# Kernel tuning notes

Measured on AMD Instinct MI355X. Metric: run time of the kernel, lower is better.

Reference implementation:

```python
import jax, jax.numpy as jnp
import numpy as np

B, C, H, W = 16, 512, 64, 64
L, D = 77, 768
NH = 8
HD = C // NH
EPS = 1e-5


def layernorm(x, g, b):
    m = jnp.mean(x, axis=-1, keepdims=True)
    v = jnp.var(x, axis=-1, keepdims=True)
    return (x - m) * jax.lax.rsqrt(v + EPS) * g + b


def setup_inputs() -> dict:
    key = jax.random.key(0)
    ks = jax.random.split(key, 12)
    s_c = 1.0 / np.sqrt(C)
    s_d = 1.0 / np.sqrt(D)
    return {
        "x": jax.random.normal(ks[0], (B, C, H, W), jnp.float32),
        "text_features": jax.random.normal(ks[1], (B, L, D), jnp.float32),
        "wq": jax.random.normal(ks[2], (C, C), jnp.float32) * s_c,
        "bq": jnp.zeros((C,), jnp.float32),
        "wk": jax.random.normal(ks[3], (C, D), jnp.float32) * s_d,
        "bk": jnp.zeros((C,), jnp.float32),
        "wv": jax.random.normal(ks[4], (C, D), jnp.float32) * s_d,
        "bv": jnp.zeros((C,), jnp.float32),
        "wo": jax.random.normal(ks[5], (C, C), jnp.float32) * s_c,
        "bo": jnp.zeros((C,), jnp.float32),
        "g1": jnp.ones((C,), jnp.float32),
        "b1": jnp.zeros((C,), jnp.float32),
        "g2": jnp.ones((C,), jnp.float32),
        "b2": jnp.zeros((C,), jnp.float32),
    }


def reference(x, text_features, wq, bq, wk, bk, wv, bv, wo, bo, g1, b1, g2, b2):
    b, c, h, w = x.shape
    # 1x1 conv query projection
    q = jnp.einsum('bchw,oc->bohw', x, wq) + bq[None, :, None, None]
    # 2D positional encoding: first c/2 channels vary along w, next c/2 along h
    pos_x = jnp.broadcast_to(jnp.linspace(0.0, 1.0, w)[None, :], (h, w))
    pos_y = jnp.broadcast_to(jnp.linspace(0.0, 1.0, h)[:, None], (h, w))
    pe = jnp.concatenate([
        jnp.broadcast_to(pos_x[None], (c // 2, h, w)),
        jnp.broadcast_to(pos_y[None], (c // 2, h, w)),
    ], axis=0)  # [C,H,W]
    q = q + 0.05 * pe[None]
    # flatten spatial -> tokens, layernorm over channels
    q_flat = q.reshape(b, c, h * w).transpose(0, 2, 1)  # [B,HW,C]
    q_norm = layernorm(q_flat, g1, b1)
    qh = q_norm.reshape(b, h * w, NH, HD)  # [B,HW,NH,HD]
    # text key/value projections
    k = jnp.einsum('bld,cd->blc', text_features, wk) + bk
    v = jnp.einsum('bld,cd->blc', text_features, wv) + bv
    k_norm = layernorm(k, g2, b2)
    kh = k_norm.reshape(b, -1, NH, HD)
    vh = v.reshape(b, -1, NH, HD)
    scale = HD ** -0.5
    attn = jnp.einsum('bqhd,bkhd->bhqk', qh, kh) * scale  # [B,NH,HW,L]
    attn = jax.nn.softmax(attn, axis=-1)  # dropout is identity in eval
    out = jnp.einsum('bhqk,bkhd->bqhd', attn, vh).reshape(b, h * w, c)
    out = out.transpose(0, 2, 1).reshape(b, c, h, w)
    out = jnp.einsum('bchw,oc->bohw', out, wo) + bo[None, :, None, None]
    return out + x
```

## Files before the change

kernel.cpp:

```cpp
#include <hip/hip_runtime.h>
#include <stdint.h>

#define BD   16
#define CD   512
#define HD_  64
#define NH_  8
#define HWD  4096
#define LD   77
#define DD   768

typedef __bf16 bf16;
typedef bf16 bf16x8 __attribute__((ext_vector_type(8)));
typedef float f32x4 __attribute__((ext_vector_type(4)));

__device__ __forceinline__ void async16(const bf16* g, bf16* l) {
  __builtin_amdgcn_global_load_lds(
      (const __attribute__((address_space(1))) void*)g,
      (__attribute__((address_space(3))) void*)l, 16, 0, 0);
}

__device__ __forceinline__ unsigned short bfb(float f) {
  bf16 h = (bf16)f;
  return __builtin_bit_cast(unsigned short, h);
}

__global__ __launch_bounds__(256) void xpose_cvt(const float* __restrict__ X,
                                                 bf16* __restrict__ Y) {
  __shared__ float tile[64][68];
  const int b = blockIdx.z, c0 = blockIdx.y * 64, t0 = blockIdx.x * 64;
  const int tid = threadIdx.x;
  const float* Xb = X + ((size_t)b * CD + c0) * HWD + t0;
#pragma unroll
  for (int p = 0; p < 4; ++p) {
    int c = (tid >> 4) + p * 16;
    int t = (tid & 15) * 4;
    float4 v = *(const float4*)(Xb + (size_t)c * HWD + t);
    *(float4*)&tile[c][t] = v;
  }
  __syncthreads();
  int t = tid >> 2, cb = (tid & 3) * 16;
  union { uint4 u[2]; unsigned short us[16]; } pk;
#pragma unroll
  for (int j = 0; j < 16; ++j) pk.us[j] = bfb(tile[cb + j][t]);
  uint4* Yp = (uint4*)(Y + ((size_t)(b * HWD + t0 + t)) * CD + c0 + cb);
  Yp[0] = pk.u[0];
  Yp[1] = pk.u[1];
}

__global__ __launch_bounds__(256) void cvt_all(
    const float* __restrict__ t, const float* __restrict__ q,
    const float* __restrict__ k, const float* __restrict__ v,
    const float* __restrict__ o, bf16* __restrict__ tb, bf16* __restrict__ qb,
    bf16* __restrict__ kb, bf16* __restrict__ vb, bf16* __restrict__ ob) {
  int bid = blockIdx.x;
  const float* src;
  bf16* dst;
  if (bid < 462) { src = t; dst = tb; }
  else if (bid < 590) { src = q; dst = qb; bid -= 462; }
  else if (bid < 782) { src = k; dst = kb; bid -= 590; }
  else if (bid < 974) { src = v; dst = vb; bid -= 782; }
  else { src = o; dst = ob; bid -= 974; }
  int i = (bid * 256 + threadIdx.x) * 8;
  float4 a = *(const float4*)(src + i);
  float4 c = *(const float4*)(src + i + 4);
  union { uint4 u; unsigned short us[8]; } pk;
  pk.us[0] = bfb(a.x); pk.us[1] = bfb(a.y); pk.us[2] = bfb(a.z); pk.us[3] = bfb(a.w);
  pk.us[4] = bfb(c.x); pk.us[5] = bfb(c.y); pk.us[6] = bfb(c.z); pk.us[7] = bfb(c.w);
  *(uint4*)(dst + i) = pk.u;
}

template <int TM, int TN, int MODE, int NBX>
__global__ __launch_bounds__(256)
void gemm_bt(const bf16* __restrict__ A, const bf16* __restrict__ B,
             int M, int N, int K,
             const float* __restrict__ bias, const float* __restrict__ xres,
             float* __restrict__ D,
             const bf16* __restrict__ B2, const float* __restrict__ bias2,
             float* __restrict__ D2) {
  constexpr int WM = TM / 2, WN = TN / 2;
  constexpr int AFR = WM / 16, BFR = WN / 16;
  constexpr int ACH = TM / 8, TCH = (TM + TN) / 8, WCH = TCH / 4;
  static_assert(WCH == 8, "vmcnt(8) literal assumes 8 loads/wave/tile");
  __shared__ bf16 sA[2][TM * 64];
  __shared__ bf16 sB[2][TN * 64];
  const int tid = threadIdx.x, wave = tid >> 6, lane = tid & 63;
  int flat = blockIdx.x;
  {
    const int qq = (int)gridDim.x >> 3;
    flat = (flat & 7) * qq + (flat >> 3);
  }
  const int m0 = (flat / NBX) * TM;
  int n0 = (flat % NBX) * TN;
  if constexpr (MODE == 2) {
    if (n0 >= (N >> 1)) { B = B2; bias = bias2; D = D2; n0 -= (N >> 1); }
  }
  const int wm = (wave >> 1) * WM, wn = (wave & 1) * WN;
  const int sub = lane >> 3, col8 = (lane & 7) * 8;
  const int mlo = lane & 15, khi = lane >> 4;
  f32x4 acc[AFR][BFR] = {};

  auto stage = [&](int buf, int k0) {
#pragma unroll
    for (int r = 0; r < WCH; ++r) {
      int ci = wave * WCH + r;
      if (ci < ACH) {
        int row = ci * 8 + sub;
        int g = m0 + row;
        if (g > M - 1) g = M - 1;
        async16(A + (size_t)g * K + k0 + col8, &sA[buf][ci * 512]);
      } else {
        int cj = ci - ACH;
        int row = cj * 8 + sub;
        async16(B + (size_t)(n0 + row) * K + k0 + col8, &sB[buf][cj * 512]);
      }
    }
  };

  const int NT = K >> 6;
  stage(0, 0);
  stage(1, 64);
  asm volatile("s_waitcnt vmcnt(8)" ::: "memory");
  __builtin_amdgcn_s_barrier();
  __builtin_amdgcn_sched_barrier(0);

  for (int t = 0; t < NT; ++t) {
    const int cur = t & 1;
#pragma unroll
    for (int kc = 0; kc < 2; ++kc) {
      bf16x8 af[AFR], bfv[BFR];
      const int ko = kc * 32 + khi * 8;
#pragma unroll
      for (int i = 0; i < AFR; ++i)
        af[i] = *(const bf16x8*)&sA[cur][(wm + i * 16 + mlo) * 64 + ko];
#pragma unroll
      for (int j = 0; j < BFR; ++j)
        bfv[j] = *(const bf16x8*)&sB[cur][(wn + j * 16 + mlo) * 64 + ko];
#pragma unroll
      for (int i = 0; i < AFR; ++i)
#pragma unroll
        for (int j = 0; j < BFR; ++j)
          acc[i][j] = __builtin_amdgcn_mfma_f32_16x16x32_bf16(af[i], bfv[j],
                                                              acc[i][j], 0, 0, 0);
    }
    asm volatile("s_waitcnt lgkmcnt(0)" ::: "memory");
    __builtin_amdgcn_s_barrier();
    if (t + 2 < NT) {
      stage(cur, (t + 2) << 6);
      asm volatile("s_waitcnt vmcnt(8)" ::: "memory");
      __builtin_amdgcn_s_barrier();
      __builtin_amdgcn_sched_barrier(0);
    } else if (t + 1 < NT) {
      asm volatile("s_waitcnt vmcnt(0)" ::: "memory");
      __builtin_amdgcn_s_barrier();
      __builtin_amdgcn_sched_barrier(0);
    }
  }

  if constexpr (MODE == 0) {
    __shared__ float sRS[TM][2][2];
    bf16* Dq = (bf16*)D;
    const int wnh = wave & 1;
#pragma unroll
    for (int i = 0; i < AFR; ++i) {
#pragma unroll
      for (int r = 0; r < 4; ++r) {
        const int rowt = wm + i * 16 + khi * 4 + r;
        const int m = m0 + rowt;
        const int hw = m & (HWD - 1);
        const float pex = (float)(hw & 63) * (0.05f / 63.0f);
        const float pey = (float)(hw >> 6) * (0.05f / 63.0f);
        float s = 0.f, sq = 0.f;
#pragma unroll
        for (int j = 0; j < BFR; ++j) {
          const int n = n0 + wn + j * 16 + mlo;
          float v = acc[i][j][r] + bias[n] + (n < 256 ? pex : pey);
          bf16 hv = (bf16)v;
          Dq[(size_t)m * CD + n] = hv;
          float vr = (float)hv;
          s += vr;
          sq += vr * vr;
        }
        s += __shfl_xor(s, 1); sq += __shfl_xor(sq, 1);
        s += __shfl_xor(s, 2); sq += __shfl_xor(sq, 2);
        s += __shfl_xor(s, 4); sq += __shfl_xor(sq, 4);
        s += __shfl_xor(s, 8); sq += __shfl_xor(sq, 8);
        if (mlo == 0) { sRS[rowt][wnh][0] = s; sRS[rowt][wnh][1] = sq; }
      }
    }
    __syncthreads();
    if (tid < TM) {
      float s = sRS[tid][0][0] + sRS[tid][1][0];
      float sq = sRS[tid][0][1] + sRS[tid][1][1];
      float2* pst = (float2*)xres;
      pst[(size_t)(n0 >> 7) * (BD * HWD) + (m0 + tid)] = make_float2(s, sq);
    }
  } else if constexpr (MODE == 3) {
    float bn[BFR];
#pragma unroll
    for (int j = 0; j < BFR; ++j) bn[j] = bias[n0 + wn + j * 16 + mlo];
#pragma unroll
    for (int i = 0; i < AFR; ++i) {
      const int m = m0 + wm + i * 16 + khi * 4;
      const int b = m >> 12, hw = m & (HWD - 1);
      const float* xr0 = xres + ((size_t)b * CD) * HWD + hw;
      float* d0 = D + ((size_t)b * CD) * HWD + hw;
#pragma unroll
      for (int j = 0; j < BFR; ++j) {
        const size_t off = (size_t)(n0 + wn + j * 16 + mlo) * HWD;
        float4 xr = *(const float4*)(xr0 + off);
        float4 ov;
        ov.x = acc[i][j][0] + bn[j] + xr.x;
        ov.y = acc[i][j][1] + bn[j] + xr.y;
        ov.z = acc[i][j][2] + bn[j] + xr.z;
        ov.w = acc[i][j][3] + bn[j] + xr.w;
        *(float4*)(d0 + off) = ov;
      }
    }
  } else {
#pragma unroll
    for (int i = 0; i < AFR; ++i) {
      const int mb = m0 + wm + i * 16 + khi * 4;
#pragma unroll
      for (int j = 0; j < BFR; ++j) {
        const int n = n0 + wn + j * 16 + mlo;
#pragma unroll
        for (int r = 0; r < 4; ++r) {
          const int m = mb + r;
          if (m < M) D[(size_t)m * CD + n] = acc[i][j][r] + bias[n];
        }
      }
    }
  }
}

__global__ __launch_bounds__(256) void ln_rows(const float* __restrict__ X,
                                               const float* __restrict__ gg,
                                               const float* __restrict__ bb,
                                               bf16* __restrict__ Y, int nrows,
                                               int khlayout) {
  const int wv = threadIdx.x >> 6, lane = threadIdx.x & 63;
  const int row = blockIdx.x * 4 + wv;
  if (row >= nrows) return;
  const float* xr = X + (size_t)row * CD + lane * 8;
  float4 v0 = *(const float4*)xr;
  float4 v1 = *(const float4*)(xr + 4);
  float xv[8] = {v0.x, v0.y, v0.z, v0.w, v1.x, v1.y, v1.z, v1.w};
  float s = 0.f, sq = 0.f;
#pragma unroll
  for (int j = 0; j < 8; ++j) { s += xv[j]; sq += xv[j] * xv[j]; }
#pragma unroll
  for (int off = 1; off < 64; off <<= 1) {
    s += __shfl_xor(s, off);
    sq += __shfl_xor(sq, off);
  }
  float mean = s * (1.0f / 512.0f);
  float var = sq * (1.0f / 512.0f) - mean * mean;
  float rstd = rsqrtf(var + 1e-5f);
  const int c0 = lane * 8;
  union { uint4 u; unsigned short us[8]; } pk;
#pragma unroll
  for (int j = 0; j < 8; ++j)
    pk.us[j] = bfb((xv[j] - mean) * rstd * gg[c0 + j] + bb[c0 + j]);
  size_t ya;
  if (khlayout) {
    int bq = row / LD, l = row - bq * LD;
    int hh = lane >> 3, dd = (lane & 7) * 8;
    ya = (((size_t)(bq * NH_ + hh)) * LD + l) * HD_ + dd;
  } else {
    ya = (size_t)row * CD + c0;
  }
  *(uint4*)(Y + ya) = pk.u;
}

__global__ __launch_bounds__(256) void make_vt(const float* __restrict__ vraw,
                                               bf16* __restrict__ vt) {
  const int bh = blockIdx.x, b = bh >> 3, h = bh & 7;
  const int tid = threadIdx.x, d = tid & 63, lg = tid >> 6;
  for (int l = lg; l < 96; l += 4) {
    float v = 0.f;
    if (l < LD) v = vraw[((size_t)(b * LD + l)) * CD + h * HD_ + d];
    vt[((size_t)(bh * HD_ + d)) * 96 + l] = (bf16)v;
  }
}

__global__ __launch_bounds__(256) void attn_k(const bf16* __restrict__ Q,
                                              const float2* __restrict__ PST,
                                              const float* __restrict__ G1,
                                              const float* __restrict__ B1,
                                              const bf16* __restrict__ KH,
                                              const bf16* __restrict__ VT,
                                              bf16* __restrict__ O) {
  __shared__ bf16 P[4][16 * 104];
  const int tid = threadIdx.x, wv = tid >> 6, lane = tid & 63;
  const int m = lane & 15, kg = lane >> 4;
  const int q0 = blockIdx.x * 64, h = blockIdx.y, b = blockIdx.z;
  const int bh = b * NH_ + h;

  const int rowg = b * HWD + q0 + wv * 16 + m;
  const size_t qoff = (size_t)rowg * CD + h * HD_;
  bf16x8 a0r = *(const bf16x8*)(Q + qoff + kg * 8);
  bf16x8 a1r = *(const bf16x8*)(Q + qoff + 32 + kg * 8);

  float2 st = PST[(size_t)kg * (BD * HWD) + rowg];
  float s = st.x, sq = st.y;
  s += __shfl_xor(s, 16); sq += __shfl_xor(sq, 16);
  s += __shfl_xor(s, 32); sq += __shfl_xor(sq, 32);
  const float mean = s * (1.0f / 512.0f);
  const float var = sq * (1.0f / 512.0f) - mean * mean;
  const float rstd = rsqrtf(var + 1e-5f);

  const int c0 = h * HD_ + kg * 8;
  float4 ga = *(const float4*)(G1 + c0), gb = *(const float4*)(G1 + c0 + 4);
  float4 gc = *(const float4*)(G1 + c0 + 32), gd = *(const float4*)(G1 + c0 + 36);
  float4 ta = *(const float4*)(B1 + c0), tb = *(const float4*)(B1 + c0 + 4);
  float4 tc = *(const float4*)(B1 + c0 + 32), td = *(const float4*)(B1 + c0 + 36);
  const float gg[16] = {ga.x, ga.y, ga.z, ga.w, gb.x, gb.y, gb.z, gb.w,
                        gc.x, gc.y, gc.z, gc.w, gd.x, gd.y, gd.z, gd.w};
  const float bbv[16] = {ta.x, ta.y, ta.z, ta.w, tb.x, tb.y, tb.z, tb.w,
                         tc.x, tc.y, tc.z, tc.w, td.x, td.y, td.z, td.w};
  bf16x8 a0, a1;
#pragma unroll
  for (int e = 0; e < 8; ++e) {
    a0[e] = (bf16)(((float)a0r[e] - mean) * rstd * gg[e] + bbv[e]);
    a1[e] = (bf16)(((float)a1r[e] - mean) * rstd * gg[8 + e] + bbv[8 + e]);
  }

  const bf16* Kb = KH + (size_t)bh * LD * HD_;
  f32x4 sacc[5];
#pragma unroll
  for (int kt = 0; kt < 5; ++kt) {
    int key = kt * 16 + m;
    if (key > LD - 1) key = LD - 1;
    const bf16* kr = Kb + key * HD_ + kg * 8;
    bf16x8 b0 = *(const bf16x8*)kr;
    bf16x8 b1 = *(const bf16x8*)(kr + 32);
    f32x4 z = {0.f, 0.f, 0.f, 0.f};
    z = __builtin_amdgcn_mfma_f32_16x16x32_bf16(a0, b0, z, 0, 0, 0);
    z = __builtin_amdgcn_mfma_f32_16x16x32_bf16(a1, b1, z, 0, 0, 0);
    sacc[kt] = z;
  }

  bf16* Pw = &P[wv][0];
#pragma unroll
  for (int r = 0; r < 4; ++r) {
    float sc[5];
#pragma unroll
    for (int kt = 0; kt < 5; ++kt) {
      float v = sacc[kt][r] * 0.125f;
      if (kt == 4 && m >= LD - 64) v = -3.0e38f;
      sc[kt] = v;
    }
    float mx = fmaxf(fmaxf(fmaxf(sc[0], sc[1]), fmaxf(sc[2], sc[3])), sc[4]);
    mx = fmaxf(mx, __shfl_xor(mx, 1));
    mx = fmaxf(mx, __shfl_xor(mx, 2));
    mx = fmaxf(mx, __shfl_xor(mx, 4));
    mx = fmaxf(mx, __shfl_xor(mx, 8));
    float sum = 0.f;
#pragma unroll
    for (int kt = 0; kt < 5; ++kt) {
      sc[kt] = __expf(sc[kt] - mx);
      sum += sc[kt];
    }
    sum += __shfl_xor(sum, 1);
    sum += __shfl_xor(sum, 2);
    sum += __shfl_xor(sum, 4);
    sum += __shfl_xor(sum, 8);
    float inv = 1.0f / sum;
    const int prow = kg * 4 + r;
#pragma unroll
    for (int kt = 0; kt < 5; ++kt)
      Pw[prow * 104 + kt * 16 + m] = (bf16)(sc[kt] * inv);
    Pw[prow * 104 + 80 + m] = (bf16)0.f;
  }
  __syncthreads();

  bf16x8 ap[3];
#pragma unroll
  for (int kc = 0; kc < 3; ++kc)
    ap[kc] = *(const bf16x8*)&Pw[m * 104 + kc * 32 + kg * 8];

  const bf16* Vb = VT + (size_t)bh * HD_ * 96;
  f32x4 o[4] = {};
#pragma unroll
  for (int nt = 0; nt < 4; ++nt) {
#pragma unroll
    for (int kc = 0; kc < 3; ++kc) {
      bf16x8 bv = *(const bf16x8*)(Vb + (nt * 16 + m) * 96 + kc * 32 + kg * 8);
      o[nt] = __builtin_amdgcn_mfma_f32_16x16x32_bf16(ap[kc], bv, o[nt], 0, 0, 0);
    }
  }
#pragma unroll
  for (int nt = 0; nt < 4; ++nt)
#pragma unroll
    for (int r = 0; r < 4; ++r) {
      const int row = b * HWD + q0 + wv * 16 + kg * 4 + r;
      O[(size_t)row * CD + h * HD_ + nt * 16 + m] = (bf16)(o[nt][r]);
    }
}

extern "C" void kernel_launch(void* const* d_in, const int* in_sizes, int n_in,
                              void* d_out, int out_size, void* d_ws, size_t ws_size,
                              hipStream_t stream) {
  const float* x    = (const float*)d_in[0];
  const float* text = (const float*)d_in[1];
  const float* wq   = (const float*)d_in[2];
  const float* bq   = (const float*)d_in[3];
  const float* wk   = (const float*)d_in[4];
  const float* bk   = (const float*)d_in[5];
  const float* wv   = (const float*)d_in[6];
  const float* bv   = (const float*)d_in[7];
  const float* wo   = (const float*)d_in[8];
  const float* bo   = (const float*)d_in[9];
  const float* g1   = (const float*)d_in[10];
  const float* b1   = (const float*)d_in[11];
  const float* g2   = (const float*)d_in[12];
  const float* b2   = (const float*)d_in[13];
  float* out = (float*)d_out;

  char* p = (char*)d_ws;
  auto alloc = [&](size_t bytes) {
    char* r = p;
    p += (bytes + 255) & ~(size_t)255;
    return r;
  };
  bf16* xt     = (bf16*)alloc((size_t)BD * HWD * CD * 2);
  bf16* attn_o = (bf16*)alloc((size_t)BD * HWD * CD * 2);
  bf16* textb  = (bf16*)alloc((size_t)BD * LD * DD * 2);
  bf16* wqb    = (bf16*)alloc((size_t)CD * CD * 2);
  bf16* wkb    = (bf16*)alloc((size_t)CD * DD * 2);
  bf16* wvb    = (bf16*)alloc((size_t)CD * DD * 2);
  bf16* wob    = (bf16*)alloc((size_t)CD * CD * 2);
  float* kraw  = (float*)alloc((size_t)BD * LD * CD * 4);
  float* vraw  = (float*)alloc((size_t)BD * LD * CD * 4);
  bf16* kh     = (bf16*)alloc((size_t)BD * NH_ * LD * HD_ * 2);
  bf16* vt     = (bf16*)alloc((size_t)BD * NH_ * HD_ * 96 * 2);
  float* pstat = (float*)alloc((size_t)4 * BD * HWD * 2 * 4);
  bf16* qbf = (bf16*)out;

  xpose_cvt<<<dim3(HWD / 64, CD / 64, BD), 256, 0, stream>>>(x, xt);
  cvt_all<<<1102, 256, 0, stream>>>(text, wq, wk, wv, wo,
                                    textb, wqb, wkb, wvb, wob);

  gemm_bt<128, 128, 2, 8><<<80, 256, 0, stream>>>(
      textb, wkb, BD * LD, 2 * CD, DD, bk, nullptr, kraw, wvb, bv, vraw);
  ln_rows<<<(BD * LD + 3) / 4, 256, 0, stream>>>(kraw, g2, b2, kh, BD * LD, 1);
  make_vt<<<BD * NH_, 256, 0, stream>>>(vraw, vt);

  gemm_bt<128, 128, 0, 4><<<2048, 256, 0, stream>>>(
      xt, wqb, BD * HWD, CD, CD, bq, pstat, (float*)qbf,
      nullptr, nullptr, nullptr);

  attn_k<<<dim3(HWD / 64, NH_, BD), 256, 0, stream>>>(
      qbf, (const float2*)pstat, g1, b1, kh, vt, attn_o);

  gemm_bt<128, 128, 3, 4><<<2048, 256, 0, stream>>>(
      attn_o, wob, BD * HWD, CD, CD, bo, x, out, nullptr, nullptr, nullptr);
}
```

Measured before the change: 539.5 us.

## Swizzle GEMM LDS tiles, precompute load pointers, fuse V transpose into GEMM epilogue

```diff
diff --git a/kernel.cpp b/kernel.cpp
--- a/kernel.cpp
+++ b/kernel.cpp
@@ -81,8 +81,7 @@
   constexpr int AFR = WM / 16, BFR = WN / 16;
   constexpr int ACH = TM / 8, TCH = (TM + TN) / 8, WCH = TCH / 4;
   static_assert(WCH == 8, "vmcnt(8) literal assumes 8 loads/wave/tile");
-  __shared__ bf16 sA[2][TM * 64];
-  __shared__ bf16 sB[2][TN * 64];
+  __shared__ bf16 sM[2][(TM + TN) * 64];
   const int tid = threadIdx.x, wave = tid >> 6, lane = tid & 63;
   int flat = blockIdx.x;
   {
@@ -91,61 +90,76 @@
   }
   const int m0 = (flat / NBX) * TM;
   int n0 = (flat % NBX) * TN;
+  bool vside = false;
   if constexpr (MODE == 2) {
-    if (n0 >= (N >> 1)) { B = B2; bias = bias2; D = D2; n0 -= (N >> 1); }
+    if (n0 >= (N >> 1)) { B = B2; bias = bias2; vside = true; n0 -= (N >> 1); }
   }
   const int wm = (wave >> 1) * WM, wn = (wave & 1) * WN;
   const int sub = lane >> 3, col8 = (lane & 7) * 8;
+  const int csw = col8 ^ (sub * 8);
   const int mlo = lane & 15, khi = lane >> 4;
+  const int rxor = (mlo & 7) * 8;
   f32x4 acc[AFR][BFR] = {};
 
-  auto stage = [&](int buf, int k0) {
-#pragma unroll
-    for (int r = 0; r < WCH; ++r) {
-      int ci = wave * WCH + r;
-      if (ci < ACH) {
-        int row = ci * 8 + sub;
-        int g = m0 + row;
-        if (g > M - 1) g = M - 1;
-        async16(A + (size_t)g * K + k0 + col8, &sA[buf][ci * 512]);
-      } else {
-        int cj = ci - ACH;
-        int row = cj * 8 + sub;
-        async16(B + (size_t)(n0 + row) * K + k0 + col8, &sB[buf][cj * 512]);
-      }
-    }
+  const bf16* gp[WCH];
+  int ldoff[WCH];
+#pragma unroll
+  for (int r = 0; r < WCH; ++r) {
+    int ci = wave * WCH + r;
+    if (ci < ACH) {
+      int g = m0 + ci * 8 + sub;
+      if (g > M - 1) g = M - 1;
+      gp[r] = A + (size_t)g * K + csw;
+      ldoff[r] = ci * 512;
+    } else {
+      int cj = ci - ACH;
+      gp[r] = B + (size_t)(n0 + cj * 8 + sub) * K + csw;
+      ldoff[r] = TM * 64 + cj * 512;
+    }
+  }
+
+  auto stage = [&](int buf, int t) {
+    const int k0 = t << 6;
+#pragma unroll
+    for (int r = 0; r < WCH; ++r)
+      async16(gp[r] + k0, &sM[buf][ldoff[r]]);
   };
 
   const int NT = K >> 6;
   stage(0, 0);
-  stage(1, 64);
+  stage(1, 1);
   asm volatile("s_waitcnt vmcnt(8)" ::: "memory");
   __builtin_amdgcn_s_barrier();
   __builtin_amdgcn_sched_barrier(0);
 
   for (int t = 0; t < NT; ++t) {
     const int cur = t & 1;
+    const bf16* sA = &sM[cur][0];
+    const bf16* sB = &sM[cur][TM * 64];
 #pragma unroll
     for (int kc = 0; kc < 2; ++kc) {
       bf16x8 af[AFR], bfv[BFR];
       const int ko = kc * 32 + khi * 8;
+      const int kos = ko ^ rxor;
 #pragma unroll
       for (int i = 0; i < AFR; ++i)
-        af[i] = *(const bf16x8*)&sA[cur][(wm + i * 16 + mlo) * 64 + ko];
+        af[i] = *(const bf16x8*)&sA[(wm + i * 16 + mlo) * 64 + kos];
 #pragma unroll
       for (int j = 0; j < BFR; ++j)
-        bfv[j] = *(const bf16x8*)&sB[cur][(wn + j * 16 + mlo) * 64 + ko];
+        bfv[j] = *(const bf16x8*)&sB[(wn + j * 16 + mlo) * 64 + kos];
+      __builtin_amdgcn_s_setprio(1);
 #pragma unroll
       for (int i = 0; i < AFR; ++i)
 #pragma unroll
         for (int j = 0; j < BFR; ++j)
           acc[i][j] = __builtin_amdgcn_mfma_f32_16x16x32_bf16(af[i], bfv[j],
                                                               acc[i][j], 0, 0, 0);
+      __builtin_amdgcn_s_setprio(0);
     }
     asm volatile("s_waitcnt lgkmcnt(0)" ::: "memory");
     __builtin_amdgcn_s_barrier();
     if (t + 2 < NT) {
-      stage(cur, (t + 2) << 6);
+      stage(cur, t + 2);
       asm volatile("s_waitcnt vmcnt(8)" ::: "memory");
       __builtin_amdgcn_s_barrier();
       __builtin_amdgcn_sched_barrier(0);
@@ -217,6 +231,7 @@
       }
     }
   } else {
+    bf16* vt = (bf16*)D2;
 #pragma unroll
     for (int i = 0; i < AFR; ++i) {
       const int mb = m0 + wm + i * 16 + khi * 4;
@@ -226,7 +241,16 @@
 #pragma unroll
         for (int r = 0; r < 4; ++r) {
           const int m = mb + r;
-          if (m < M) D[(size_t)m * CD + n] = acc[i][j][r] + bias[n];
+          if (m < M) {
+            float v = acc[i][j][r] + bias[n];
+            if (!vside) {
+              D[(size_t)m * CD + n] = v;
+            } else {
+              const int b = m / LD, l = m - b * LD;
+              const int h = n >> 6, d = n & 63;
+              vt[(((size_t)(b * NH_ + h)) * HD_ + d) * 96 + l] = (bf16)v;
+            }
+          }
         }
       }
     }
@@ -236,8 +260,7 @@
 __global__ __launch_bounds__(256) void ln_rows(const float* __restrict__ X,
                                                const float* __restrict__ gg,
                                                const float* __restrict__ bb,
-                                               bf16* __restrict__ Y, int nrows,
-                                               int khlayout) {
+                                               bf16* __restrict__ Y, int nrows) {
   const int wv = threadIdx.x >> 6, lane = threadIdx.x & 63;
   const int row = blockIdx.x * 4 + wv;
   if (row >= nrows) return;
@@ -261,26 +284,10 @@
 #pragma unroll
   for (int j = 0; j < 8; ++j)
     pk.us[j] = bfb((xv[j] - mean) * rstd * gg[c0 + j] + bb[c0 + j]);
-  size_t ya;
-  if (khlayout) {
-    int bq = row / LD, l = row - bq * LD;
-    int hh = lane >> 3, dd = (lane & 7) * 8;
-    ya = (((size_t)(bq * NH_ + hh)) * LD + l) * HD_ + dd;
-  } else {
-    ya = (size_t)row * CD + c0;
-  }
+  int bq = row / LD, l = row - bq * LD;
+  int hh = lane >> 3, dd = (lane & 7) * 8;
+  size_t ya = (((size_t)(bq * NH_ + hh)) * LD + l) * HD_ + dd;
   *(uint4*)(Y + ya) = pk.u;
-}
-
-__global__ __launch_bounds__(256) void make_vt(const float* __restrict__ vraw,
-                                               bf16* __restrict__ vt) {
-  const int bh = blockIdx.x, b = bh >> 3, h = bh & 7;
-  const int tid = threadIdx.x, d = tid & 63, lg = tid >> 6;
-  for (int l = lg; l < 96; l += 4) {
-    float v = 0.f;
-    if (l < LD) v = vraw[((size_t)(b * LD + l)) * CD + h * HD_ + d];
-    vt[((size_t)(bh * HD_ + d)) * 96 + l] = (bf16)v;
-  }
 }
 
 __global__ __launch_bounds__(256) void attn_k(const bf16* __restrict__ Q,
@@ -431,20 +438,19 @@
   bf16* wvb    = (bf16*)alloc((size_t)CD * DD * 2);
   bf16* wob    = (bf16*)alloc((size_t)CD * CD * 2);
   float* kraw  = (float*)alloc((size_t)BD * LD * CD * 4);
-  float* vraw  = (float*)alloc((size_t)BD * LD * CD * 4);
   bf16* kh     = (bf16*)alloc((size_t)BD * NH_ * LD * HD_ * 2);
   bf16* vt     = (bf16*)alloc((size_t)BD * NH_ * HD_ * 96 * 2);
   float* pstat = (float*)alloc((size_t)4 * BD * HWD * 2 * 4);
   bf16* qbf = (bf16*)out;
 
+  hipMemsetAsync(vt, 0, (size_t)BD * NH_ * HD_ * 96 * 2, stream);
   xpose_cvt<<<dim3(HWD / 64, CD / 64, BD), 256, 0, stream>>>(x, xt);
   cvt_all<<<1102, 256, 0, stream>>>(text, wq, wk, wv, wo,
                                     textb, wqb, wkb, wvb, wob);
 
   gemm_bt<128, 128, 2, 8><<<80, 256, 0, stream>>>(
-      textb, wkb, BD * LD, 2 * CD, DD, bk, nullptr, kraw, wvb, bv, vraw);
-  ln_rows<<<(BD * LD + 3) / 4, 256, 0, stream>>>(kraw, g2, b2, kh, BD * LD, 1);
-  make_vt<<<BD * NH_, 256, 0, stream>>>(vraw, vt);
+      textb, wkb, BD * LD, 2 * CD, DD, bk, nullptr, kraw, wvb, bv, (float*)vt);
+  ln_rows<<<(BD * LD + 3) / 4, 256, 0, stream>>>(kraw, g2, b2, kh, BD * LD);
 
   gemm_bt<128, 128, 0, 4><<<2048, 256, 0, stream>>>(
       xt, wqb, BD * HWD, CD, CD, bq, pstat, (float*)qbf,
```

Result: faster. 524.6 us (-2.8%).
